# Optimization experiments

Hardware: AMD Instinct MI355X
Metric: run time of the kernel (lower is better)

Reference implementation:

```python
import jax, jax.numpy as jnp
import numpy as np

RMS_EPS = 1e-5


def setup_inputs() -> dict:
    key = jax.random.key(0)
    ks = jax.random.split(key, 7)
    B, N, D, H = 8, 1024, 1024, 4
    Dv = D // H
    s = lambda k, shp, fan: jax.random.normal(k, shp, jnp.float32) * (1.0 / np.sqrt(fan))
    return {
        "x": jax.random.normal(ks[0], (B, N, D), jnp.float32),
        "Wq": s(ks[1], (D, D), D),
        "Wk": s(ks[2], (D, D), D),
        "Wv": s(ks[3], (D, D), D),
        "Wbeta": s(ks[4], (D, H), D),
        "Wo": s(ks[5], (D, D), D),
        "g_norm": jnp.ones((Dv,), jnp.float32),
    }


def _l2norm(t):
    return t / jnp.linalg.norm(t, axis=-1, keepdims=True)


def _delta_rule(q, k, v, beta):
    # q,k: [B,H,N,Dk]; v: [B,H,N,Dv]; beta: [B,H,N]
    B, H, N, Dk = q.shape
    Dv = v.shape[-1]
    # time-major for scan: [N,B,H,D]
    qT = jnp.moveaxis(q, 2, 0)
    kT = jnp.moveaxis(k, 2, 0)
    vT = jnp.moveaxis(v, 2, 0)
    bT = jnp.moveaxis(beta, 2, 0)  # [N,B,H]

    def step(S, inp):
        q_t, k_t, v_t, b_t = inp  # [B,H,Dk], [B,H,Dk], [B,H,Dv], [B,H]
        pred = jnp.einsum('bhk,bhkv->bhv', k_t, S)
        err = (v_t - pred) * b_t[..., None]          # delta-rule error, scaled by beta
        S = S + jnp.einsum('bhk,bhv->bhkv', k_t, err)  # rank-1 state update
        o_t = jnp.einsum('bhk,bhkv->bhv', q_t, S)
        return S, o_t

    S0 = jnp.zeros((B, H, Dk, Dv), q.dtype)
    _, oT = jax.lax.scan(step, S0, (qT, kT, vT, bT))
    return jnp.moveaxis(oT, 0, 2)  # [B,H,N,Dv]


def reference(x, Wq, Wk, Wv, Wbeta, Wo, g_norm):
    B, N, D = x.shape
    H = Wbeta.shape[1]
    Dk = Wq.shape[1] // H
    Dv = Wv.shape[1] // H
    split = lambda t, d: t.reshape(B, N, H, d).transpose(0, 2, 1, 3)  # b n (h d) -> b h n d
    q = _l2norm(split(x @ Wq, Dk))
    k = _l2norm(split(x @ Wk, Dk))
    v = split(x @ Wv, Dv)
    beta = jax.nn.sigmoid(x @ Wbeta).transpose(0, 2, 1)  # [B,H,N]
    o = _delta_rule(q, k, v, beta)  # [B,H,N,Dv]
    # per-head RMSNorm over Dv
    o = o * jax.lax.rsqrt(jnp.mean(o * o, axis=-1, keepdims=True) + RMS_EPS) * g_norm
    o = o.transpose(0, 2, 1, 3).reshape(B, N, H * Dv)  # b h n d -> b n (h d)
    return o @ Wo
```

## Files before the change

### kernel.cpp

```cpp
#include <hip/hip_runtime.h>
#include <hip/hip_bf16.h>
#include <math.h>

typedef unsigned short u16;
typedef __attribute__((ext_vector_type(8))) __bf16 bf16x8;
typedef __attribute__((ext_vector_type(4))) float f32x4;

#define MFMA16 __builtin_amdgcn_mfma_f32_16x16x32_bf16

__device__ __forceinline__ float bf2f(unsigned int u) {
    union { unsigned int i; float f; } x;
    x.i = (u & 0xffffu) << 16;
    return x.f;
}
__device__ __forceinline__ u16 f2bf(float f) {
    unsigned int i = __float_as_uint(f);
    unsigned int r = (i + 0x7fffu + ((i >> 16) & 1u)) >> 16;
    return (u16)r;
}

__device__ __forceinline__ void gload_lds16(const void* g, void* l) {
    __builtin_amdgcn_global_load_lds((const __attribute__((address_space(1))) void*)g,
                                     (__attribute__((address_space(3))) void*)l, 16, 0, 0);
}

#define BARS() do { asm volatile("s_waitcnt lgkmcnt(0)" ::: "memory"); \
                    __builtin_amdgcn_s_barrier(); } while (0)

__global__ void detect_dtype(const unsigned* __restrict__ wq, int* __restrict__ flag)
{
    int lane = threadIdx.x;
    unsigned lo = wq[lane] & 0xffffu;
    unsigned e = (lo >> 7) & 0xffu;
    int m = (e >= 0x6e && e <= 0x7e) ? 1 : 0;
#pragma unroll
    for (int s = 1; s < 64; s <<= 1) m += __shfl_xor(m, s);
    if (lane == 0) flag[0] = (m >= 32) ? 0 : 1;
}

__global__ __launch_bounds__(256) void convert_vec4(
    const void* __restrict__ src, u16* __restrict__ dst, int nchunk, const int* __restrict__ flag)
{
    int stride = gridDim.x * 256;
    int i0 = blockIdx.x * 256 + threadIdx.x;
    if (*flag) {
        const float4* s = (const float4*)src;
        for (int i = i0; i < nchunk; i += stride) {
            float4 v = s[i];
            ushort4 o;
            o.x = f2bf(v.x); o.y = f2bf(v.y); o.z = f2bf(v.z); o.w = f2bf(v.w);
            *(ushort4*)(dst + (size_t)i * 4) = o;
        }
    } else {
        const uint2* s = (const uint2*)src;
        uint2* d = (uint2*)dst;
        for (int i = i0; i < nchunk; i += stride) d[i] = s[i];
    }
}

__global__ __launch_bounds__(256) void transpose_cvt(
    const void* __restrict__ w0, const void* __restrict__ w1,
    const void* __restrict__ w2, const void* __restrict__ w3,
    u16* __restrict__ o0, u16* __restrict__ o1,
    u16* __restrict__ o2, u16* __restrict__ o3, const int* __restrict__ flag)
{
    const void* in; u16* out;
    switch (blockIdx.z) {
        case 0: in = w0; out = o0; break;
        case 1: in = w1; out = o1; break;
        case 2: in = w2; out = o2; break;
        default: in = w3; out = o3; break;
    }
    int n  = blockIdx.x * 64 + (threadIdx.x & 63);
    int kb = blockIdx.y * 32 + (threadIdx.x >> 6) * 8;
    u16 v[8];
    if (*flag) {
        const float* f = (const float*)in;
#pragma unroll
        for (int j = 0; j < 8; ++j) v[j] = f2bf(f[(size_t)(kb + j) * 1024 + n]);
    } else {
        const u16* s = (const u16*)in;
#pragma unroll
        for (int j = 0; j < 8; ++j) v[j] = s[(size_t)(kb + j) * 1024 + n];
    }
    uint4 pk;
    pk.x = (unsigned)v[0] | ((unsigned)v[1] << 16);
    pk.y = (unsigned)v[2] | ((unsigned)v[3] << 16);
    pk.z = (unsigned)v[4] | ((unsigned)v[5] << 16);
    pk.w = (unsigned)v[6] | ((unsigned)v[7] << 16);
    *(uint4*)(out + (size_t)n * 1024 + kb) = pk;
}

__global__ __launch_bounds__(256) void gemm_bt(
    const u16* __restrict__ A, const u16* __restrict__ BT, void* __restrict__ C,
    int M, int Nn, int K, const int* __restrict__ flag, int fp32_out)
{
    __shared__ alignas(16) u16 As[128 * 32];
    __shared__ alignas(16) u16 Bs[128 * 32];
    const int tid  = threadIdx.x;
    const int lane = tid & 63;
    const int wv   = tid >> 6;
    const int wm   = wv >> 1, wn = wv & 1;
    const int bm   = blockIdx.x * 128, bn = blockIdx.y * 128;
    const int fr   = lane & 15, fk = lane >> 4;

    f32x4 acc[4][4];
#pragma unroll
    for (int i = 0; i < 4; ++i)
#pragma unroll
        for (int j = 0; j < 4; ++j) acc[i][j] = (f32x4){0.f, 0.f, 0.f, 0.f};

    for (int k0 = 0; k0 < K; k0 += 32) {
        __syncthreads();
#pragma unroll
        for (int p = 0; p < 2; ++p) {
            int i = tid + p * 256;
            int r = i >> 2, kc = (i & 3) << 3;
            gload_lds16(A  + (size_t)(bm + r) * K + k0 + kc,
                        (char*)As + (size_t)(wv * 64 + p * 256) * 16);
            gload_lds16(BT + (size_t)(bn + r) * K + k0 + kc,
                        (char*)Bs + (size_t)(wv * 64 + p * 256) * 16);
        }
        __syncthreads();
        bf16x8 af[4], bfr[4];
#pragma unroll
        for (int mi = 0; mi < 4; ++mi)
            af[mi] = *(const bf16x8*)(As + (wm * 64 + mi * 16 + fr) * 32 + fk * 8);
#pragma unroll
        for (int ni = 0; ni < 4; ++ni)
            bfr[ni] = *(const bf16x8*)(Bs + (wn * 64 + ni * 16 + fr) * 32 + fk * 8);
#pragma unroll
        for (int mi = 0; mi < 4; ++mi)
#pragma unroll
            for (int ni = 0; ni < 4; ++ni)
                acc[mi][ni] = MFMA16(af[mi], bfr[ni], acc[mi][ni], 0, 0, 0);
    }
    bool f32st = fp32_out && (*flag);
    if (f32st) {
        float* Cf = (float*)C;
#pragma unroll
        for (int mi = 0; mi < 4; ++mi)
#pragma unroll
            for (int ni = 0; ni < 4; ++ni)
#pragma unroll
                for (int j = 0; j < 4; ++j) {
                    int row = bm + wm * 64 + mi * 16 + fk * 4 + j;
                    int col = bn + wn * 64 + ni * 16 + fr;
                    Cf[(size_t)row * Nn + col] = acc[mi][ni][j];
                }
    } else {
        u16* Cb = (u16*)C;
#pragma unroll
        for (int mi = 0; mi < 4; ++mi)
#pragma unroll
            for (int ni = 0; ni < 4; ++ni)
#pragma unroll
                for (int j = 0; j < 4; ++j) {
                    int row = bm + wm * 64 + mi * 16 + fk * 4 + j;
                    int col = bn + wn * 64 + ni * 16 + fr;
                    Cb[(size_t)row * Nn + col] = f2bf(acc[mi][ni][j]);
                }
    }
}

__global__ __launch_bounds__(256) void gemm_qkv(
    const u16* __restrict__ A, const u16* __restrict__ BT,
    u16* __restrict__ Qo, u16* __restrict__ Ko, u16* __restrict__ Vo)
{
    __shared__ alignas(16) u16 As[128 * 32];
    __shared__ alignas(16) u16 Bs[128 * 32];
    const int tid  = threadIdx.x;
    const int lane = tid & 63;
    const int wv   = tid >> 6;
    const int wm   = wv >> 1, wn = wv & 1;
    const int bm   = blockIdx.x * 128, bn = blockIdx.y * 128;
    const int fr   = lane & 15, fk = lane >> 4;

    f32x4 acc[4][4];
#pragma unroll
    for (int i = 0; i < 4; ++i)
#pragma unroll
        for (int j = 0; j < 4; ++j) acc[i][j] = (f32x4){0.f, 0.f, 0.f, 0.f};

    for (int k0 = 0; k0 < 1024; k0 += 32) {
        __syncthreads();
#pragma unroll
        for (int p = 0; p < 2; ++p) {
            int i = tid + p * 256;
            int r = i >> 2, kc = (i & 3) << 3;
            gload_lds16(A  + (size_t)(bm + r) * 1024 + k0 + kc,
                        (char*)As + (size_t)(wv * 64 + p * 256) * 16);
            gload_lds16(BT + (size_t)(bn + r) * 1024 + k0 + kc,
                        (char*)Bs + (size_t)(wv * 64 + p * 256) * 16);
        }
        __syncthreads();
        bf16x8 af[4], bfr[4];
#pragma unroll
        for (int mi = 0; mi < 4; ++mi)
            af[mi] = *(const bf16x8*)(As + (wm * 64 + mi * 16 + fr) * 32 + fk * 8);
#pragma unroll
        for (int ni = 0; ni < 4; ++ni)
            bfr[ni] = *(const bf16x8*)(Bs + (wn * 64 + ni * 16 + fr) * 32 + fk * 8);
#pragma unroll
        for (int mi = 0; mi < 4; ++mi)
#pragma unroll
            for (int ni = 0; ni < 4; ++ni)
                acc[mi][ni] = MFMA16(af[mi], bfr[ni], acc[mi][ni], 0, 0, 0);
    }
    const int seg = bn >> 10;
    u16* Cb = (seg == 0) ? Qo : (seg == 1) ? Ko : Vo;
    const int cb = bn & 1023;
#pragma unroll
    for (int mi = 0; mi < 4; ++mi)
#pragma unroll
        for (int ni = 0; ni < 4; ++ni)
#pragma unroll
            for (int j = 0; j < 4; ++j) {
                int row = bm + wm * 64 + mi * 16 + fk * 4 + j;
                int col = cb + wn * 64 + ni * 16 + fr;
                Cb[(size_t)row * 1024 + col] = f2bf(acc[mi][ni][j]);
            }
}

__global__ __launch_bounds__(256) void beta_kernel(
    const u16* __restrict__ x, const void* __restrict__ Wbv,
    float* __restrict__ beta, const int* __restrict__ flag)
{
    int row  = blockIdx.x * 4 + (threadIdx.x >> 6);
    int lane = threadIdx.x & 63;
    const u16* xr = x + (size_t)row * 1024;
    float a0 = 0.f, a1 = 0.f, a2 = 0.f, a3 = 0.f;
    if (*flag) {
        const float4* wf = (const float4*)Wbv;
        for (int c = 0; c < 16; ++c) {
            int k = c * 64 + lane;
            float xv = bf2f(xr[k]);
            float4 w = wf[k];
            a0 += xv * w.x; a1 += xv * w.y; a2 += xv * w.z; a3 += xv * w.w;
        }
    } else {
        const u16* wb = (const u16*)Wbv;
        for (int c = 0; c < 16; ++c) {
            int k = c * 64 + lane;
            float xv = bf2f(xr[k]);
            uint2 w = *(const uint2*)(wb + (size_t)k * 4);
            a0 += xv * bf2f(w.x);
            a1 += xv * bf2f(w.x >> 16);
            a2 += xv * bf2f(w.y);
            a3 += xv * bf2f(w.y >> 16);
        }
    }
#pragma unroll
    for (int m = 1; m < 64; m <<= 1) {
        a0 += __shfl_xor(a0, m); a1 += __shfl_xor(a1, m);
        a2 += __shfl_xor(a2, m); a3 += __shfl_xor(a3, m);
    }
    if (lane == 0) {
        int b = row >> 10, nn = row & 1023;
        beta[(size_t)(b * 4 + 0) * 1024 + nn] = 1.f / (1.f + expf(-a0));
        beta[(size_t)(b * 4 + 1) * 1024 + nn] = 1.f / (1.f + expf(-a1));
        beta[(size_t)(b * 4 + 2) * 1024 + nn] = 1.f / (1.f + expf(-a2));
        beta[(size_t)(b * 4 + 3) * 1024 + nn] = 1.f / (1.f + expf(-a3));
    }
}

#define AP 65
__global__ __launch_bounds__(256, 2) void phaseA(
    u16* Kb, u16* Qb,
    const float* __restrict__ Bp,
    u16* __restrict__ M1hi, u16* __restrict__ M1lo,
    u16* KTg)
{
    const int bh = blockIdx.x >> 4, ch = blockIdx.x & 15;
    const int bq = bh >> 2, h = bh & 3;
    const int tid = threadIdx.x;
    const int w = tid >> 6, L = tid & 63, fr = L & 15, fk = L >> 4;

    __shared__ alignas(16) u16 Ks[64 * 264];
    __shared__ alignas(16) u16 Qs[64 * 264];
    __shared__ float bc[64];

    float* Af = (float*)Ks;
    float* Tf = (float*)(Ks + 8320);
    u16* TtH = Qs;
    u16* TtL = Qs + 64 * 72;
    u16* QKs = Qs + 2 * 64 * 72;

    const size_t crow = ((size_t)bq * 1024 + ch * 64) * 1024 + (size_t)h * 256;
#pragma unroll
    for (int i = 0; i < 8; ++i) {
        int row = i * 8 + (tid >> 5), c8 = (tid & 31) * 8;
        const size_t ga = crow + (size_t)row * 1024 + c8;
        union { uint4 q; u16 u[8]; } KV, QV;
        KV.q = *(const uint4*)(Kb + ga);
        QV.q = *(const uint4*)(Qb + ga);
        float kf[8], qf[8], ssk = 0.f, ssq = 0.f;
#pragma unroll
        for (int e = 0; e < 8; ++e) {
            kf[e] = bf2f(KV.u[e]); ssk += kf[e] * kf[e];
            qf[e] = bf2f(QV.u[e]); ssq += qf[e] * qf[e];
        }
#pragma unroll
        for (int m = 1; m < 32; m <<= 1) {
            ssk += __shfl_xor(ssk, m);
            ssq += __shfl_xor(ssq, m);
        }
        float rk = rsqrtf(ssk + 1e-20f), rq = rsqrtf(ssq + 1e-20f);
#pragma unroll
        for (int e = 0; e < 8; ++e) {
            KV.u[e] = f2bf(kf[e] * rk);
            QV.u[e] = f2bf(qf[e] * rq);
        }
        *(uint4*)(Ks + row * 264 + c8) = KV.q;
        *(uint4*)(Qs + row * 264 + c8) = QV.q;
        *(uint4*)(Kb + ga) = KV.q;
        *(uint4*)(Qb + ga) = QV.q;
    }
    if (tid < 64) bc[tid] = Bp[(size_t)bh * 1024 + ch * 64 + tid];
    __syncthreads();

    const size_t kbase = (size_t)(bh * 16 + ch) * 16384;
#pragma unroll
    for (int i = 0; i < 8; ++i) {
        int item = tid + i * 256;
        int t = item & 63, g = item >> 6;
        union { uint4 q; u16 u[8]; } U;
        U.q = *(const uint4*)(Ks + t * 264 + g * 8);
#pragma unroll
        for (int e = 0; e < 8; ++e)
            KTg[kbase + (size_t)(g * 8 + e) * 64 + t] = U.u[e];
    }

    f32x4 kk[4], qk[4];
#pragma unroll
    for (int n = 0; n < 4; ++n) { kk[n] = (f32x4){0,0,0,0}; qk[n] = (f32x4){0,0,0,0}; }
#pragma unroll
    for (int k0 = 0; k0 < 8; ++k0) {
        bf16x8 ak = *(const bf16x8*)(Ks + (w * 16 + fr) * 264 + k0 * 32 + fk * 8);
        bf16x8 aq = *(const bf16x8*)(Qs + (w * 16 + fr) * 264 + k0 * 32 + fk * 8);
#pragma unroll
        for (int n = 0; n < 4; ++n) {
            bf16x8 bk = *(const bf16x8*)(Ks + (n * 16 + fr) * 264 + k0 * 32 + fk * 8);
            kk[n] = MFMA16(ak, bk, kk[n], 0, 0, 0);
            qk[n] = MFMA16(aq, bk, qk[n], 0, 0, 0);
        }
    }
    __syncthreads();

#pragma unroll
    for (int n = 0; n < 4; ++n)
#pragma unroll
        for (int j = 0; j < 4; ++j) {
            int t = w * 16 + fk * 4 + j, s = n * 16 + fr;
            Af[t * AP + s] = (s < t) ? bc[t] * kk[n][j] : 0.f;
            QKs[t * 72 + s] = f2bf((s <= t) ? qk[n][j] : 0.f);
        }
    for (int i = tid; i < 64 * AP; i += 256) Tf[i] = 0.f;
    __syncthreads();

    {
        int j = w * 16 + fr;
        int p = fk;
        for (int t = 0; t < 64; ++t) {
            float acc = 0.f;
#pragma unroll
            for (int i = 0; i < 16; ++i) {
                int s = p + 4 * i;
                acc += Af[t * AP + s] * Tf[s * AP + j];
            }
            acc += __shfl_xor(acc, 16);
            acc += __shfl_xor(acc, 32);
            float val = ((t == j) ? 1.f : 0.f) - acc;
            if (p == 0) Tf[t * AP + j] = val;
        }
    }
    __syncthreads();

#pragma unroll
    for (int e = 0; e < 16; ++e) {
        int idx = tid + e * 256;
        int t = idx >> 6, s = idx & 63;
        float f = Tf[t * AP + s];
        u16 hh = f2bf(f);
        TtH[s * 72 + t] = hh;
        TtL[s * 72 + t] = f2bf(f - bf2f(hh));
    }
    __syncthreads();

    const size_t tb2 = (size_t)(bh * 16 + ch) * 4096;
    f32x4 accM[4];
#pragma unroll
    for (int ns = 0; ns < 4; ++ns) accM[ns] = (f32x4){0,0,0,0};
#pragma unroll
    for (int k0 = 0; k0 < 2; ++k0) {
        bf16x8 aq = *(const bf16x8*)(QKs + (w * 16 + fr) * 72 + k0 * 32 + fk * 8);
#pragma unroll
        for (int ns = 0; ns < 4; ++ns) {
            bf16x8 bh_ = *(const bf16x8*)(TtH + (ns * 16 + fr) * 72 + k0 * 32 + fk * 8);
            bf16x8 bl_ = *(const bf16x8*)(TtL + (ns * 16 + fr) * 72 + k0 * 32 + fk * 8);
            accM[ns] = MFMA16(aq, bh_, accM[ns], 0, 0, 0);
            accM[ns] = MFMA16(aq, bl_, accM[ns], 0, 0, 0);
        }
    }
#pragma unroll
    for (int ns = 0; ns < 4; ++ns)
#pragma unroll
        for (int j = 0; j < 4; ++j) {
            int t = w * 16 + fk * 4 + j, a = ns * 16 + fr;
            float v = accM[ns][j];
            u16 hh = f2bf(v);
            M1hi[tb2 + t * 64 + a] = hh;
            M1lo[tb2 + t * 64 + a] = f2bf(v - bf2f(hh));
        }

    asm volatile("s_waitcnt vmcnt(0)" ::: "memory");
#pragma unroll
    for (int nn = 0; nn < 4; ++nn) {
        bf16x8 af2[2];
#pragma unroll
        for (int k0 = 0; k0 < 2; ++k0)
            af2[k0] = *(const bf16x8*)(KTg + kbase
                        + (size_t)(w * 64 + nn * 16 + fr) * 64 + k0 * 32 + fk * 8);
        f32x4 acc2[4];
#pragma unroll
        for (int ns = 0; ns < 4; ++ns) acc2[ns] = (f32x4){0,0,0,0};
#pragma unroll
        for (int k0 = 0; k0 < 2; ++k0)
#pragma unroll
            for (int ns = 0; ns < 4; ++ns) {
                bf16x8 bh_ = *(const bf16x8*)(TtH + (ns * 16 + fr) * 72 + k0 * 32 + fk * 8);
                bf16x8 bl_ = *(const bf16x8*)(TtL + (ns * 16 + fr) * 72 + k0 * 32 + fk * 8);
                acc2[ns] = MFMA16(af2[k0], bh_, acc2[ns], 0, 0, 0);
                acc2[ns] = MFMA16(af2[k0], bl_, acc2[ns], 0, 0, 0);
            }
        asm volatile("s_waitcnt vmcnt(0)" ::: "memory");
#pragma unroll
        for (int ns = 0; ns < 4; ++ns)
#pragma unroll
            for (int j = 0; j < 4; ++j)
                KTg[kbase + (size_t)(w * 64 + nn * 16 + fk * 4 + j) * 64 + ns * 16 + fr]
                    = f2bf(acc2[ns][j]);
    }
}

#define WTP 72
#define SHP 264
__global__ __launch_bounds__(256, 1) void phaseB(
    const u16* __restrict__ Kb, const u16* __restrict__ Qb, u16* Vb,
    const float* __restrict__ Bp,
    const u16* __restrict__ M1hi, const u16* __restrict__ M1lo,
    const u16* __restrict__ Ktil)
{
    const int bh  = blockIdx.x & 31;
    const int dvb = blockIdx.x >> 5;
    const int bq = bh >> 2, h = bh & 3;
    const int tid = threadIdx.x;
    const int w = tid >> 6, L = tid & 63, fr = L & 15, fk = L >> 4;
    const int rl = L >> 5, cp = L & 31;

    __shared__ alignas(16) u16 Kl[64 * 256];
    __shared__ alignas(16) u16 Ql[64 * 256];
    __shared__ alignas(16) u16 S_hi[32 * SHP];
    __shared__ alignas(16) u16 S_lo[32 * SHP];
    __shared__ alignas(16) u16 W_T[32 * WTP];
    __shared__ float bc[1024];

    for (int i = tid; i < 32 * SHP; i += 256) { S_hi[i] = 0; S_lo[i] = 0; }
    for (int i = tid; i < 1024; i += 256) bc[i] = Bp[(size_t)bh * 1024 + i];

    const size_t rb = ((size_t)bq * 1024) * 1024 + (size_t)h * 256;

    f32x4 sreg[2][4];
#pragma unroll
    for (int n = 0; n < 2; ++n)
#pragma unroll
        for (int nn = 0; nn < 4; ++nn) sreg[n][nn] = (f32x4){0,0,0,0};

    bf16x8 m1h[2], m1l[2], ktf[2][4];
    u16 vr[2][4];

    auto stage_kq = [&](int c) {
        const size_t crow = rb + (size_t)(c * 64) * 1024;
#pragma unroll
        for (int i = 0; i < 8; ++i) {
            int rg = w * 16 + 2 * i + rl;
            int cu = cp ^ (rg & 7);
            gload_lds16(Kb + crow + (size_t)rg * 1024 + cu * 8,
                        (char*)Kl + (size_t)(w * 16 + 2 * i) * 512);
            gload_lds16(Qb + crow + (size_t)rg * 1024 + cu * 8,
                        (char*)Ql + (size_t)(w * 16 + 2 * i) * 512);
        }
    };
    auto pf_m1 = [&](int c) {
        const size_t mb = (size_t)(bh * 16 + c) * 4096 + (size_t)(w * 16 + fr) * 64 + fk * 8;
#pragma unroll
        for (int k0 = 0; k0 < 2; ++k0) {
            m1h[k0] = *(const bf16x8*)(M1hi + mb + k0 * 32);
            m1l[k0] = *(const bf16x8*)(M1lo + mb + k0 * 32);
        }
    };
    auto pf_ktf = [&](int c) {
        const size_t kb2 = (size_t)(bh * 16 + c) * 16384;
#pragma unroll
        for (int k0 = 0; k0 < 2; ++k0)
#pragma unroll
            for (int nn = 0; nn < 4; ++nn)
                ktf[k0][nn] = *(const bf16x8*)(Ktil + kb2
                              + (size_t)(w * 64 + nn * 16 + fr) * 64 + k0 * 32 + fk * 8);
    };
    auto pf_vr = [&](int c) {
        const size_t crow = rb + (size_t)(c * 64) * 1024;
#pragma unroll
        for (int n = 0; n < 2; ++n)
#pragma unroll
            for (int j = 0; j < 4; ++j)
                vr[n][j] = Vb[crow + (size_t)(w * 16 + fk * 4 + j) * 1024
                              + dvb * 32 + n * 16 + fr];
    };

    stage_kq(0); pf_m1(0); pf_ktf(0); pf_vr(0);
    __syncthreads();

    for (int c = 0; c < 16; ++c) {
        asm volatile("s_waitcnt vmcnt(0)" ::: "memory");
        f32x4 aPh[2], aPl[2], aOh[2], aOl[2];
#pragma unroll
        for (int n = 0; n < 2; ++n) {
            aPh[n] = (f32x4){0,0,0,0}; aPl[n] = (f32x4){0,0,0,0};
            aOh[n] = (f32x4){0,0,0,0}; aOl[n] = (f32x4){0,0,0,0};
        }
#pragma unroll
        for (int k0 = 0; k0 < 8; ++k0) {
            int ru = ((k0 * 4 + fk) ^ (fr & 7)) * 8;
            bf16x8 kqf = *(const bf16x8*)(Kl + (w * 16 + fr) * 256 + ru);
            bf16x8 qqf = *(const bf16x8*)(Ql + (w * 16 + fr) * 256 + ru);
#pragma unroll
            for (int n = 0; n < 2; ++n) {
                bf16x8 shi = *(const bf16x8*)(S_hi + (n * 16 + fr) * SHP + k0 * 32 + fk * 8);
                bf16x8 slo = *(const bf16x8*)(S_lo + (n * 16 + fr) * SHP + k0 * 32 + fk * 8);
                aPh[n] = MFMA16(kqf, shi, aPh[n], 0, 0, 0);
                aPl[n] = MFMA16(kqf, slo, aPl[n], 0, 0, 0);
                aOh[n] = MFMA16(qqf, shi, aOh[n], 0, 0, 0);
                aOl[n] = MFMA16(qqf, slo, aOl[n], 0, 0, 0);
            }
        }
        const size_t crow = rb + (size_t)(c * 64) * 1024;
#pragma unroll
        for (int n = 0; n < 2; ++n) {
            f32x4 accP = aPh[n] + aPl[n];
#pragma unroll
            for (int j = 0; j < 4; ++j) {
                int t = w * 16 + fk * 4 + j;
                W_T[(n * 16 + fr) * WTP + t] = f2bf(bc[c * 64 + t] * (bf2f(vr[n][j]) - accP[j]));
            }
        }
        if (c + 1 < 16) stage_kq(c + 1);
        BARS();
        bf16x8 wf[2][2];
#pragma unroll
        for (int n = 0; n < 2; ++n)
#pragma unroll
            for (int k0 = 0; k0 < 2; ++k0)
                wf[n][k0] = *(const bf16x8*)(W_T + (n * 16 + fr) * WTP + k0 * 32 + fk * 8);
        f32x4 accO[2];
#pragma unroll
        for (int n = 0; n < 2; ++n) {
            accO[n] = aOh[n] + aOl[n];
#pragma unroll
            for (int k0 = 0; k0 < 2; ++k0) {
                accO[n] = MFMA16(m1h[k0], wf[n][k0], accO[n], 0, 0, 0);
                accO[n] = MFMA16(m1l[k0], wf[n][k0], accO[n], 0, 0, 0);
            }
#pragma unroll
            for (int j = 0; j < 4; ++j)
                Vb[crow + (size_t)(w * 16 + fk * 4 + j) * 1024 + dvb * 32 + n * 16 + fr]
                    = f2bf(accO[n][j]);
        }
        if (c + 1 < 16) pf_m1(c + 1);
        f32x4 dS[2][4];
#pragma unroll
        for (int n = 0; n < 2; ++n)
#pragma unroll
            for (int nn = 0; nn < 4; ++nn) dS[n][nn] = (f32x4){0,0,0,0};
#pragma unroll
        for (int k0 = 0; k0 < 2; ++k0)
#pragma unroll
            for (int n = 0; n < 2; ++n)
#pragma unroll
                for (int nn = 0; nn < 4; ++nn)
                    dS[n][nn] = MFMA16(wf[n][k0], ktf[k0][nn], dS[n][nn], 0, 0, 0);
        if (c + 1 < 16) { pf_ktf(c + 1); pf_vr(c + 1); }
#pragma unroll
        for (int n = 0; n < 2; ++n)
#pragma unroll
            for (int nn = 0; nn < 4; ++nn) {
                sreg[n][nn] = sreg[n][nn] + dS[n][nn];
#pragma unroll
                for (int j = 0; j < 4; ++j) {
                    int idx = (n * 16 + fk * 4 + j) * SHP + (w * 64 + nn * 16 + fr);
                    float s = sreg[n][nn][j];
                    u16 hh = f2bf(s);
                    S_hi[idx] = hh;
                    S_lo[idx] = f2bf(s - bf2f(hh));
                }
            }
        BARS();
    }
}

__global__ __launch_bounds__(256) void rmsnorm_o(
    u16* V, const void* __restrict__ gnv, const int* __restrict__ flag)
{
    int w    = blockIdx.x * 4 + (threadIdx.x >> 6);
    int lane = threadIdx.x & 63;
    u16* p = V + (size_t)(w >> 2) * 1024 + (w & 3) * 256 + lane * 4;
    uint2 u = *(const uint2*)p;
    float f0 = bf2f(u.x), f1 = bf2f(u.x >> 16), f2 = bf2f(u.y), f3 = bf2f(u.y >> 16);
    float ss = f0 * f0 + f1 * f1 + f2 * f2 + f3 * f3;
#pragma unroll
    for (int m = 1; m < 64; m <<= 1) ss += __shfl_xor(ss, m);
    float sc = rsqrtf(ss * (1.0f / 256.0f) + 1e-5f);
    int d0 = lane * 4;
    float g0, g1, g2, g3;
    if (*flag) {
        float4 g4 = ((const float4*)gnv)[lane];
        g0 = g4.x; g1 = g4.y; g2 = g4.z; g3 = g4.w;
    } else {
        uint2 gu = *(const uint2*)((const u16*)gnv + d0);
        g0 = bf2f(gu.x); g1 = bf2f(gu.x >> 16); g2 = bf2f(gu.y); g3 = bf2f(gu.y >> 16);
    }
    uint2 o;
    o.x = (unsigned)f2bf(f0 * sc * g0) | ((unsigned)f2bf(f1 * sc * g1) << 16);
    o.y = (unsigned)f2bf(f2 * sc * g2) | ((unsigned)f2bf(f3 * sc * g3) << 16);
    *(uint2*)p = o;
}

extern "C" void kernel_launch(void* const* d_in, const int* in_sizes, int n_in,
                              void* d_out, int out_size, void* d_ws, size_t ws_size,
                              hipStream_t stream)
{
    const void* x  = d_in[0];
    const void* Wq = d_in[1];
    const void* Wk = d_in[2];
    const void* Wv = d_in[3];
    const void* Wb = d_in[4];
    const void* Wo = d_in[5];
    const void* gn = d_in[6];

    char* ws = (char*)d_ws;
    const size_t OFF_FLAG = 0;
    const size_t OFF_XB   = OFF_FLAG + 16384;
    const size_t OFF_WQT  = OFF_XB + 16777216;
    const size_t OFF_WKT  = OFF_WQT + 2097152;
    const size_t OFF_WVT  = OFF_WKT + 2097152;
    const size_t OFF_WOT  = OFF_WVT + 2097152;
    const size_t OFF_Q    = OFF_WOT + 2097152;
    const size_t OFF_K    = OFF_Q + 16777216;
    const size_t OFF_V    = OFF_K + 16777216;
    const size_t OFF_BP   = OFF_V + 16777216;

    const size_t OFF_M1H  = OFF_XB + 8388608;
    const size_t OFF_M1L  = OFF_XB + 12582912;

    int*   flag = (int*)(ws + OFF_FLAG);
    u16*   Xb   = (u16*)(ws + OFF_XB);
    u16*   wqT  = (u16*)(ws + OFF_WQT);
    u16*   wkT  = (u16*)(ws + OFF_WKT);
    u16*   wvT  = (u16*)(ws + OFF_WVT);
    u16*   woT  = (u16*)(ws + OFF_WOT);
    u16*   Qb   = (u16*)(ws + OFF_Q);
    u16*   Kb   = (u16*)(ws + OFF_K);
    u16*   Vb   = (u16*)(ws + OFF_V);
    float* Bp   = (float*)(ws + OFF_BP);
    u16*   M1hi = (u16*)(ws + OFF_M1H);
    u16*   M1lo = (u16*)(ws + OFF_M1L);
    u16*   KTg  = (u16*)d_out;

    detect_dtype<<<1, 64, 0, stream>>>((const unsigned*)Wq, flag);
    convert_vec4<<<2048, 256, 0, stream>>>(x, Xb, 2097152, flag);
    transpose_cvt<<<dim3(16, 32, 4), 256, 0, stream>>>(Wq, Wk, Wv, Wo, wqT, wkT, wvT, woT, flag);

    gemm_qkv<<<dim3(64, 24), 256, 0, stream>>>(Xb, wqT, Qb, Kb, Vb);
    beta_kernel<<<2048, 256, 0, stream>>>(Xb, Wb, Bp, flag);

    phaseA<<<512, 256, 0, stream>>>(Kb, Qb, Bp, M1hi, M1lo, KTg);
    phaseB<<<256, 256, 0, stream>>>(Kb, Qb, Vb, Bp, M1hi, M1lo, KTg);

    rmsnorm_o<<<8192, 256, 0, stream>>>(Vb, gn, flag);
    gemm_bt<<<dim3(64, 8), 256, 0, stream>>>(Vb, woT, d_out, 8192, 1024, 1024, flag, 1);
}
```

Before: 242.9 us.

## Double GEMM K-tile to 64 with XOR-swizzled LDS layout

Both bf16 GEMM kernels (generic and fused QKV) now stage 64-wide K slices per iteration instead of 32. This halves the number of barrier pairs and loop iterations. An XOR swizzle of the 16-byte column chunk by row index is applied on the global-to-LDS load and on the fragment reads, which is meant to avoid LDS bank conflicts on the 128-byte row stride. LDS use per block doubles to 32 KB, which may reduce occupancy.

```diff
diff --git a/kernel.cpp b/kernel.cpp
--- a/kernel.cpp
+++ b/kernel.cpp
@@ -95,14 +95,16 @@
     const u16* __restrict__ A, const u16* __restrict__ BT, void* __restrict__ C,
     int M, int Nn, int K, const int* __restrict__ flag, int fp32_out)
 {
-    __shared__ alignas(16) u16 As[128 * 32];
-    __shared__ alignas(16) u16 Bs[128 * 32];
+    __shared__ alignas(16) u16 As[128 * 64];
+    __shared__ alignas(16) u16 Bs[128 * 64];
     const int tid  = threadIdx.x;
     const int lane = tid & 63;
     const int wv   = tid >> 6;
     const int wm   = wv >> 1, wn = wv & 1;
     const int bm   = blockIdx.x * 128, bn = blockIdx.y * 128;
     const int fr   = lane & 15, fk = lane >> 4;
+    const int scol = ((lane & 7) ^ ((lane >> 3) & 7)) * 8;
+    const int rsub = lane >> 3;
 
     f32x4 acc[4][4];
 #pragma unroll
@@ -110,30 +112,38 @@
 #pragma unroll
         for (int j = 0; j < 4; ++j) acc[i][j] = (f32x4){0.f, 0.f, 0.f, 0.f};
 
-    for (int k0 = 0; k0 < K; k0 += 32) {
+    for (int k0 = 0; k0 < K; k0 += 64) {
         __syncthreads();
 #pragma unroll
-        for (int p = 0; p < 2; ++p) {
-            int i = tid + p * 256;
-            int r = i >> 2, kc = (i & 3) << 3;
-            gload_lds16(A  + (size_t)(bm + r) * K + k0 + kc,
-                        (char*)As + (size_t)(wv * 64 + p * 256) * 16);
-            gload_lds16(BT + (size_t)(bn + r) * K + k0 + kc,
-                        (char*)Bs + (size_t)(wv * 64 + p * 256) * 16);
+        for (int j = 0; j < 4; ++j) {
+            int row = wv * 8 + j * 32 + rsub;
+            gload_lds16(A  + (size_t)(bm + row) * K + k0 + scol,
+                        (char*)As + (size_t)(wv * 64 + j * 256) * 16);
+            gload_lds16(BT + (size_t)(bn + row) * K + k0 + scol,
+                        (char*)Bs + (size_t)(wv * 64 + j * 256) * 16);
         }
         __syncthreads();
-        bf16x8 af[4], bfr[4];
-#pragma unroll
-        for (int mi = 0; mi < 4; ++mi)
-            af[mi] = *(const bf16x8*)(As + (wm * 64 + mi * 16 + fr) * 32 + fk * 8);
-#pragma unroll
-        for (int ni = 0; ni < 4; ++ni)
-            bfr[ni] = *(const bf16x8*)(Bs + (wn * 64 + ni * 16 + fr) * 32 + fk * 8);
-#pragma unroll
-        for (int mi = 0; mi < 4; ++mi)
-#pragma unroll
-            for (int ni = 0; ni < 4; ++ni)
-                acc[mi][ni] = MFMA16(af[mi], bfr[ni], acc[mi][ni], 0, 0, 0);
+#pragma unroll
+        for (int kk0 = 0; kk0 < 2; ++kk0) {
+            bf16x8 af[4], bfr[4];
+#pragma unroll
+            for (int mi = 0; mi < 4; ++mi) {
+                int R = wm * 64 + mi * 16 + fr;
+                int u = (kk0 * 4 + fk) ^ (R & 7);
+                af[mi] = *(const bf16x8*)(As + (size_t)R * 64 + u * 8);
+            }
+#pragma unroll
+            for (int ni = 0; ni < 4; ++ni) {
+                int R = wn * 64 + ni * 16 + fr;
+                int u = (kk0 * 4 + fk) ^ (R & 7);
+                bfr[ni] = *(const bf16x8*)(Bs + (size_t)R * 64 + u * 8);
+            }
+#pragma unroll
+            for (int mi = 0; mi < 4; ++mi)
+#pragma unroll
+                for (int ni = 0; ni < 4; ++ni)
+                    acc[mi][ni] = MFMA16(af[mi], bfr[ni], acc[mi][ni], 0, 0, 0);
+        }
     }
     bool f32st = fp32_out && (*flag);
     if (f32st) {
@@ -167,14 +177,16 @@
     const u16* __restrict__ A, const u16* __restrict__ BT,
     u16* __restrict__ Qo, u16* __restrict__ Ko, u16* __restrict__ Vo)
 {
-    __shared__ alignas(16) u16 As[128 * 32];
-    __shared__ alignas(16) u16 Bs[128 * 32];
+    __shared__ alignas(16) u16 As[128 * 64];
+    __shared__ alignas(16) u16 Bs[128 * 64];
     const int tid  = threadIdx.x;
     const int lane = tid & 63;
     const int wv   = tid >> 6;
     const int wm   = wv >> 1, wn = wv & 1;
     const int bm   = blockIdx.x * 128, bn = blockIdx.y * 128;
     const int fr   = lane & 15, fk = lane >> 4;
+    const int scol = ((lane & 7) ^ ((lane >> 3) & 7)) * 8;
+    const int rsub = lane >> 3;
 
     f32x4 acc[4][4];
 #pragma unroll
@@ -182,30 +194,38 @@
 #pragma unroll
         for (int j = 0; j < 4; ++j) acc[i][j] = (f32x4){0.f, 0.f, 0.f, 0.f};
 
-    for (int k0 = 0; k0 < 1024; k0 += 32) {
+    for (int k0 = 0; k0 < 1024; k0 += 64) {
         __syncthreads();
 #pragma unroll
-        for (int p = 0; p < 2; ++p) {
-            int i = tid + p * 256;
-            int r = i >> 2, kc = (i & 3) << 3;
-            gload_lds16(A  + (size_t)(bm + r) * 1024 + k0 + kc,
-                        (char*)As + (size_t)(wv * 64 + p * 256) * 16);
-            gload_lds16(BT + (size_t)(bn + r) * 1024 + k0 + kc,
-                        (char*)Bs + (size_t)(wv * 64 + p * 256) * 16);
+        for (int j = 0; j < 4; ++j) {
+            int row = wv * 8 + j * 32 + rsub;
+            gload_lds16(A  + (size_t)(bm + row) * 1024 + k0 + scol,
+                        (char*)As + (size_t)(wv * 64 + j * 256) * 16);
+            gload_lds16(BT + (size_t)(bn + row) * 1024 + k0 + scol,
+                        (char*)Bs + (size_t)(wv * 64 + j * 256) * 16);
         }
         __syncthreads();
-        bf16x8 af[4], bfr[4];
-#pragma unroll
-        for (int mi = 0; mi < 4; ++mi)
-            af[mi] = *(const bf16x8*)(As + (wm * 64 + mi * 16 + fr) * 32 + fk * 8);
-#pragma unroll
-        for (int ni = 0; ni < 4; ++ni)
-            bfr[ni] = *(const bf16x8*)(Bs + (wn * 64 + ni * 16 + fr) * 32 + fk * 8);
-#pragma unroll
-        for (int mi = 0; mi < 4; ++mi)
-#pragma unroll
-            for (int ni = 0; ni < 4; ++ni)
-                acc[mi][ni] = MFMA16(af[mi], bfr[ni], acc[mi][ni], 0, 0, 0);
+#pragma unroll
+        for (int kk0 = 0; kk0 < 2; ++kk0) {
+            bf16x8 af[4], bfr[4];
+#pragma unroll
+            for (int mi = 0; mi < 4; ++mi) {
+                int R = wm * 64 + mi * 16 + fr;
+                int u = (kk0 * 4 + fk) ^ (R & 7);
+                af[mi] = *(const bf16x8*)(As + (size_t)R * 64 + u * 8);
+            }
+#pragma unroll
+            for (int ni = 0; ni < 4; ++ni) {
+                int R = wn * 64 + ni * 16 + fr;
+                int u = (kk0 * 4 + fk) ^ (R & 7);
+                bfr[ni] = *(const bf16x8*)(Bs + (size_t)R * 64 + u * 8);
+            }
+#pragma unroll
+            for (int mi = 0; mi < 4; ++mi)
+#pragma unroll
+                for (int ni = 0; ni < 4; ++ni)
+                    acc[mi][ni] = MFMA16(af[mi], bfr[ni], acc[mi][ni], 0, 0, 0);
+        }
     }
     const int seg = bn >> 10;
     u16* Cb = (seg == 0) ? Qo : (seg == 1) ? Ko : Vo;
```

Result: faster. 234.3 us, median of 2 (-3.5%).
